# Kernel tuning notes

Hardware: AMD Instinct MI355X
Metric: run time of the kernel (lower is better)

The kernel has to match this reference:

```python
import jax, jax.numpy as jnp
import numpy as np

K_POOL = 5

def _conv_lookahead(x, W):
    # Faithful to F.conv2d(pad=(fs//2+1,0)) followed by keeping the last L rows:
    # for fs=3 this reduces to out[t] = sum_j x[t+j] @ W[:,j,:].T (2 trailing zeros).
    # x: [..., L, E], W: [nf, fs, E] -> out [..., L, nf]
    fs = W.shape[1]
    L = x.shape[-2]
    pad = [(0, 0)] * (x.ndim - 2) + [(0, fs - 1), (0, 0)]
    xp = jnp.pad(x, pad)
    out = sum(jnp.einsum('...le,fe->...lf', jax.lax.dynamic_slice_in_dim(xp, j, L, axis=-2), W[:, j, :]) for j in range(fs))
    return out

def _cosine(q, s):
    # q: [B,Q,D], s: [B,S,L,D] -> [B,S,Q,L]
    num = jnp.einsum('bqd,bsld->bsql', q, s)
    qn = jnp.linalg.norm(q, axis=-1)  # [B,Q]
    sn = jnp.linalg.norm(s, axis=-1)  # [B,S,L]
    return num / (qn[:, None, :, None] * sn[:, :, None, :])

def _pool(sim, k=K_POOL):
    # sort-based k-max pooling over last dim -> (max, mean-of-top-k), matching torch.sort + slice
    top = jax.lax.top_k(sim, k)[0]            # [..., Q, k] descending
    return jnp.stack([top[..., 0], top.mean(-1)], axis=-1)  # [..., Q, 2]

def _bce(p, t):
    return -(t * jnp.log(p) + (1.0 - t) * jnp.log(1.0 - p)).mean()

def setup_inputs() -> dict:
    key = jax.random.key(0)
    ks = jax.random.split(key, 9)
    B, S, L, Q, V, E, NF, FS = 16, 48, 64, 32, 50000, 300, 256, 3
    return {
        'sentences': jax.random.randint(ks[0], (B, S, L), 0, V, dtype=jnp.int64 if jax.config.jax_enable_x64 else jnp.int32).astype(jnp.int32),
        'question': jax.random.randint(ks[1], (B, Q), 0, V).astype(jnp.int32),
        'target_sents': jax.random.randint(ks[2], (B, S), 0, 2).astype(jnp.int32),
        'target_docs': jax.random.randint(ks[3], (B,), 0, 2).astype(jnp.int32),
        'similarity_one_hot': jax.random.uniform(ks[4], (B, S, Q, L), dtype=jnp.float32),
        'embeds': jax.random.normal(ks[5], (V, E), dtype=jnp.float32),
        'conv_w': jax.random.normal(ks[6], (NF, FS, E), dtype=jnp.float32),
        'lin_w': jax.random.normal(ks[7], (1, 6), dtype=jnp.float32),
        'lin_b': jax.random.normal(ks[8], (1,), dtype=jnp.float32),
    }

def reference(sentences, question, target_sents, target_docs, similarity_one_hot, embeds, conv_w, lin_w, lin_b):
    q_emb = embeds[question]            # [B,Q,E]
    s_emb = embeds[sentences]           # [B,S,L,E]
    q_conv = _conv_lookahead(q_emb, conv_w)   # [B,Q,NF]
    s_conv = _conv_lookahead(s_emb, conv_w)   # [B,S,L,NF]

    sim_ins = _cosine(q_emb, s_emb)     # [B,S,Q,L]
    qmask = (question > 1).astype(sim_ins.dtype)   # [B,Q]
    smask = (sentences > 1).astype(sim_ins.dtype)  # [B,S,L]
    sim_ins = sim_ins * qmask[:, None, :, None] * smask[:, :, None, :]

    sim_sens = _cosine(q_conv, s_conv)  # [B,S,Q,L]

    feats = jnp.concatenate([_pool(sim_ins), _pool(sim_sens), _pool(similarity_one_hot)], axis=-1)  # [B,S,Q,6]
    lo = jax.nn.sigmoid(jnp.einsum('bsqf,of->bsqo', feats, lin_w)[..., 0] + lin_b[0])  # [B,S,Q]
    sent_output = lo.mean(-1)           # [B,S]

    sal = _bce(sent_output, target_sents.astype(sent_output.dtype))
    doc_emit = sent_output.max(-1)      # [B]
    dal = _bce(doc_emit, target_docs.astype(doc_emit.dtype))
    total_loss = (sal + dal) / 2.0
    return (total_loss, sent_output, doc_emit)
```

## Files before the change

### kernel.cpp

```cpp
#include <hip/hip_runtime.h>
#include <math.h>

#define NB 16
#define NS 48
#define NL 64
#define NQ 32
#define NE 300
#define NF 256
#define KP 320
#define QROWS 36

typedef __attribute__((ext_vector_type(8))) short short8;
typedef __attribute__((ext_vector_type(4))) float f32x4;

#define MFMA(a,b,c) __builtin_amdgcn_mfma_f32_16x16x32_bf16((a),(b),(c),0,0,0)

__device__ __forceinline__ unsigned short f2bf(float f) {
    unsigned u = __float_as_uint(f);
    u += 0x7fff + ((u >> 16) & 1);
    return (unsigned short)(u >> 16);
}

__device__ __forceinline__ float wave_reduce_sum(float v) {
#pragma unroll
    for (int off = 32; off; off >>= 1) v += __shfl_xor(v, off, 64);
    return v;
}

__device__ __forceinline__ void top5_pool4(float v0, float v1, float v2, float v3,
                                           int lane, float* mx, float* mn) {
    float s0 = 0.f, s1 = 0.f, s2 = 0.f, s3 = 0.f;
    float x0 = 0.f, x1 = 0.f, x2 = 0.f, x3 = 0.f;
#pragma unroll
    for (int i = 0; i < 5; ++i) {
        float m0 = v0, m1 = v1, m2 = v2, m3 = v3;
#pragma unroll
        for (int off = 32; off; off >>= 1) {
            m0 = fmaxf(m0, __shfl_xor(m0, off, 64));
            m1 = fmaxf(m1, __shfl_xor(m1, off, 64));
            m2 = fmaxf(m2, __shfl_xor(m2, off, 64));
            m3 = fmaxf(m3, __shfl_xor(m3, off, 64));
        }
        if (i == 0) { x0 = m0; x1 = m1; x2 = m2; x3 = m3; }
        s0 += m0; s1 += m1; s2 += m2; s3 += m3;
        unsigned long long k0 = __ballot(v0 == m0);
        unsigned long long k1 = __ballot(v1 == m1);
        unsigned long long k2 = __ballot(v2 == m2);
        unsigned long long k3 = __ballot(v3 == m3);
        if (lane == __ffsll(k0) - 1) v0 = -3.4e38f;
        if (lane == __ffsll(k1) - 1) v1 = -3.4e38f;
        if (lane == __ffsll(k2) - 1) v2 = -3.4e38f;
        if (lane == __ffsll(k3) - 1) v3 = -3.4e38f;
    }
    mx[0] = x0; mx[1] = x1; mx[2] = x2; mx[3] = x3;
    mn[0] = s0 * 0.2f; mn[1] = s1 * 0.2f; mn[2] = s2 * 0.2f; mn[3] = s3 * 0.2f;
}

__global__ void wb2_kernel(const float* __restrict__ conv_w, short8* __restrict__ Wb2,
                           unsigned int* __restrict__ done_ctr,
                           float* __restrict__ qcssq) {
    if (blockIdx.x == 0 && threadIdx.x == 0) done_ctr[0] = 0u;
    int i = blockIdx.x * 256 + threadIdx.x;
    if (i < NB * NQ) qcssq[i] = 0.f;
    if (i >= 120 * 256) return;
    int rl = i & 15;
    int ftile = (i >> 4) & 15;
    int c = i >> 8;
    int kg = c & 3, rest = c >> 2;
    int ks = rest % 10, j = rest / 10;
    int f = ftile * 16 + rl;
    int k0 = ks * 32 + kg * 8;
    const float* src = conv_w + (size_t)(f * 3 + j) * NE;
    short8 h;
#pragma unroll
    for (int e = 0; e < 8; ++e) {
        int k = k0 + e;
        h[e] = (short)((k < NE) ? f2bf(src[k]) : (unsigned short)0);
    }
    Wb2[i] = h;
}

__global__ void qe_kernel(const int* __restrict__ question, const float* __restrict__ embeds,
                          unsigned short* __restrict__ qe, short8* __restrict__ qef,
                          float* __restrict__ q_norm) {
    int row = blockIdx.x;
    int b = row / QROWS, r = row % QROWS;
    int l = threadIdx.x;
    unsigned short* dst = qe + (size_t)row * KP;
    if (r < NQ) {
        int tok = question[b * NQ + r];
        const float4* rp = (const float4*)(embeds + (size_t)tok * NE);
        short8 h = {0, 0, 0, 0, 0, 0, 0, 0};
        float ss = 0.f;
        if (l < 38) {
            float4 v0 = rp[2 * l];
            ss += v0.x * v0.x + v0.y * v0.y + v0.z * v0.z + v0.w * v0.w;
            h[0] = (short)f2bf(v0.x); h[1] = (short)f2bf(v0.y);
            h[2] = (short)f2bf(v0.z); h[3] = (short)f2bf(v0.w);
            if (2 * l + 1 < 75) {
                float4 v1 = rp[2 * l + 1];
                ss += v1.x * v1.x + v1.y * v1.y + v1.z * v1.z + v1.w * v1.w;
                h[4] = (short)f2bf(v1.x); h[5] = (short)f2bf(v1.y);
                h[6] = (short)f2bf(v1.z); h[7] = (short)f2bf(v1.w);
            }
        }
        if (l < 40) {
            *(short8*)(dst + 8 * l) = h;
            qef[((size_t)(b * 2 + (r >> 4)) * 40 + l) * 16 + (r & 15)] = h;
        }
        ss = wave_reduce_sum(ss);
        if (l == 0) q_norm[b * NQ + r] = sqrtf(ss);
    } else {
        if (l < 40) {
            short8 z = {0, 0, 0, 0, 0, 0, 0, 0};
            *(short8*)(dst + 8 * l) = z;
        }
    }
}

__global__ __launch_bounds__(256) void qconv_mfma_kernel(
        const unsigned short* __restrict__ qe, const short8* __restrict__ Wb2,
        short8* __restrict__ qcf, float* __restrict__ qcssq) {
    __shared__ unsigned short tile[NQ][72];
    int b = blockIdx.x >> 2, fq = blockIdx.x & 3;
    int tid = threadIdx.x, lane = tid & 63, w = tid >> 6;
    int rl = lane & 15, kg = lane >> 4;
    int ftile = fq * 4 + w;
    f32x4 acc0 = (f32x4){0.f, 0.f, 0.f, 0.f};
    f32x4 acc1 = (f32x4){0.f, 0.f, 0.f, 0.f};
    for (int j = 0; j < 3; ++j) {
#pragma unroll 2
        for (int ks = 0; ks < 10; ++ks) {
            int k = ks * 32 + kg * 8;
            int c = (j * 10 + ks) * 4 + kg;
            short8 a0 = *(const short8*)(qe + ((size_t)(b * QROWS) + rl + j) * KP + k);
            short8 a1 = *(const short8*)(qe + ((size_t)(b * QROWS) + 16 + rl + j) * KP + k);
            short8 bb = Wb2[(c * 16 + ftile) * 16 + rl];
            acc0 = MFMA(a0, bb, acc0);
            acc1 = MFMA(a1, bb, acc1);
        }
    }
    int fl = w * 16 + rl;
#pragma unroll
    for (int reg = 0; reg < 4; ++reg) {
        tile[kg * 4 + reg][fl] = f2bf(acc0[reg]);
        tile[16 + kg * 4 + reg][fl] = f2bf(acc1[reg]);
    }
    __syncthreads();
    {
        int mh = tid >> 7, c_local = (tid >> 4) & 7, rl2 = tid & 15;
        short8 h = *(const short8*)(&tile[mh * 16 + rl2][c_local * 8]);
        qcf[((size_t)(b * 2 + mh) * 32 + 8 * fq + c_local) * 16 + rl2] = h;
    }
    {
        int qq = tid >> 3, fgrp = tid & 7;
        short8 h = *(const short8*)(&tile[qq][fgrp * 8]);
        float ss = 0.f;
#pragma unroll
        for (int e = 0; e < 8; ++e) {
            float v = __uint_as_float(((unsigned)(unsigned short)h[e]) << 16);
            ss += v * v;
        }
        ss += __shfl_xor(ss, 1, 64);
        ss += __shfl_xor(ss, 2, 64);
        ss += __shfl_xor(ss, 4, 64);
        if (fgrp == 0) atomicAdd(&qcssq[b * NQ + qq], ss);
    }
}

__global__ __launch_bounds__(256) void pack_kernel(
        const int* __restrict__ sentences, const float* __restrict__ embeds,
        short8* __restrict__ sB, float* __restrict__ snorm_g,
        float* __restrict__ scssq) {
    __shared__ unsigned short stg[16][328];
    __shared__ int toks[NL];
    int bs = blockIdx.x;
    int tid = threadIdx.x, lane = tid & 63, w = tid >> 6;
    if (tid < NL) {
        toks[tid] = sentences[(size_t)bs * NL + tid];
        scssq[bs * NL + tid] = 0.f;
    }
    __syncthreads();
    short8* sbb = sB + (size_t)bs * 40 * 64;
    for (int it = 0; it < 4; ++it) {
#pragma unroll
        for (int i = 0; i < 4; ++i) {
            int r16 = w * 4 + i;
            int r = it * 16 + r16;
            const float4* rp = (const float4*)(embeds + (size_t)toks[r] * NE);
            float ss;
            {
                float4 v = rp[lane];
                ss = v.x * v.x + v.y * v.y + v.z * v.z + v.w * v.w;
                ushort4 h = {f2bf(v.x), f2bf(v.y), f2bf(v.z), f2bf(v.w)};
                *(ushort4*)&stg[r16][4 * lane] = h;
            }
            if (lane < 11) {
                float4 v = rp[64 + lane];
                ss += v.x * v.x + v.y * v.y + v.z * v.z + v.w * v.w;
                ushort4 h = {f2bf(v.x), f2bf(v.y), f2bf(v.z), f2bf(v.w)};
                *(ushort4*)&stg[r16][256 + 4 * lane] = h;
            } else if (lane < 16) {
                ushort4 z = {0, 0, 0, 0};
                *(ushort4*)&stg[r16][256 + 4 * lane] = z;
            }
            ss = wave_reduce_sum(ss);
            if (lane == 0) snorm_g[bs * NL + r] = sqrtf(ss);
        }
        __syncthreads();
        {
            int c = tid >> 4, rl = tid & 15;
            for (; c < 40; c += 16) {
                short8 h = *(const short8*)&stg[rl][c * 8];
                sbb[(size_t)c * 64 + it * 16 + rl] = h;
            }
        }
        __syncthreads();
    }
}

__global__ __launch_bounds__(256) void ins_kernel(
        const int* __restrict__ sentences, const int* __restrict__ question,
        const short8* __restrict__ sB, const short8* __restrict__ qef,
        const float* __restrict__ snorm_g, const float* __restrict__ q_norm,
        float2* __restrict__ fpool_ins) {
    __shared__ float sim[NQ][66];
    __shared__ float qn_s[NQ], qmf_s[NQ];
    int bs = blockIdx.x, b = bs / NS;
    int tid = threadIdx.x, lane = tid & 63, w = tid >> 6;
    int rl = lane & 15, kg = lane >> 4;
    int t = (w << 4) + rl;
    if (tid < NQ) qn_s[tid] = q_norm[b * NQ + tid];
    else if (tid < 2 * NQ) {
        int q = tid - NQ;
        qmf_s[q] = (question[b * NQ + q] > 1) ? 1.f : 0.f;
    }
    float sn_t = snorm_g[bs * NL + t];
    float sm_t = (sentences[(size_t)bs * NL + t] > 1) ? 1.f : 0.f;
    __syncthreads();
    f32x4 i0 = (f32x4){0.f, 0.f, 0.f, 0.f};
    f32x4 i1 = (f32x4){0.f, 0.f, 0.f, 0.f};
    const short8* qf = qef + (size_t)(b * 80) * 16;
    const short8* sbb = sB + (size_t)bs * 40 * 64;
#pragma unroll 2
    for (int ks = 0; ks < 10; ++ks) {
        int c = ks * 4 + kg;
        short8 bB = sbb[(size_t)c * 64 + t];
        i0 = MFMA(qf[c * 16 + rl], bB, i0);
        i1 = MFMA(qf[(40 + c) * 16 + rl], bB, i1);
    }
    float inv_t = sm_t / sn_t;
#pragma unroll
    for (int reg = 0; reg < 4; ++reg) {
        int q0 = kg * 4 + reg;
        sim[q0][t] = i0[reg] / qn_s[q0] * inv_t * qmf_s[q0];
        int q1 = 16 + kg * 4 + reg;
        sim[q1][t] = i1[reg] / qn_s[q1] * inv_t * qmf_s[q1];
    }
    __syncthreads();
    int q0 = w << 3;
    float mx[4], mn[4];
    top5_pool4(sim[q0 + 0][lane], sim[q0 + 1][lane], sim[q0 + 2][lane], sim[q0 + 3][lane],
               lane, mx, mn);
    if (lane == 0)
#pragma unroll
        for (int p = 0; p < 4; ++p)
            fpool_ins[(size_t)bs * NQ + q0 + p] = (float2){mx[p], mn[p]};
    top5_pool4(sim[q0 + 4][lane], sim[q0 + 5][lane], sim[q0 + 6][lane], sim[q0 + 7][lane],
               lane, mx, mn);
    if (lane == 0)
#pragma unroll
        for (int p = 0; p < 4; ++p)
            fpool_ins[(size_t)bs * NQ + q0 + 4 + p] = (float2){mx[p], mn[p]};
}

__global__ __launch_bounds__(256) void conv_kernel(
        const short8* __restrict__ sB, const short8* __restrict__ Wb2,
        short8* __restrict__ scB, float* __restrict__ scssq) {
    __shared__ unsigned short scr[4][16][68];
    int bs = blockIdx.x;
    int tid = threadIdx.x, lane = tid & 63, w = tid >> 6;
    int rl = lane & 15, kg = lane >> 4;
    const short8* sbb = sB + (size_t)bs * 40 * 64;

    f32x4 cacc[4][4];
#pragma unroll
    for (int m = 0; m < 4; ++m)
#pragma unroll
        for (int nn = 0; nn < 4; ++nn) cacc[m][nn] = (f32x4){0.f, 0.f, 0.f, 0.f};

    for (int j = 0; j < 3; ++j) {
#pragma unroll 2
        for (int ks = 0; ks < 10; ++ks) {
            int cA = ks * 4 + kg;
            int c = (j * 10 + ks) * 4 + kg;
            short8 a[4], bb[4];
#pragma unroll
            for (int m = 0; m < 3; ++m)
                a[m] = sbb[(size_t)cA * 64 + m * 16 + rl + j];
            {
                int row3 = 48 + rl + j;
                short8 z = {0, 0, 0, 0, 0, 0, 0, 0};
                a[3] = (row3 < 64) ? sbb[(size_t)cA * 64 + row3] : z;
            }
#pragma unroll
            for (int nn = 0; nn < 4; ++nn)
                bb[nn] = Wb2[(c * 16 + (w * 4 + nn)) * 16 + rl];
#pragma unroll
            for (int m = 0; m < 4; ++m)
#pragma unroll
                for (int nn = 0; nn < 4; ++nn)
                    cacc[m][nn] = MFMA(a[m], bb[nn], cacc[m][nn]);
        }
    }

    short8* scb = scB + (size_t)bs * 32 * 64;
#pragma unroll
    for (int m = 0; m < 4; ++m) {
#pragma unroll
        for (int nn = 0; nn < 4; ++nn)
#pragma unroll
            for (int reg = 0; reg < 4; ++reg)
                scr[w][kg * 4 + reg][nn * 16 + rl] = f2bf(cacc[m][nn][reg]);
#pragma unroll
        for (int reg = 0; reg < 4; ++reg) {
            float ss = 0.f;
#pragma unroll
            for (int nn = 0; nn < 4; ++nn) {
                float v = cacc[m][nn][reg];
                ss += v * v;
            }
            ss += __shfl_xor(ss, 1, 64);
            ss += __shfl_xor(ss, 2, 64);
            ss += __shfl_xor(ss, 4, 64);
            ss += __shfl_xor(ss, 8, 64);
            if (rl == 0) atomicAdd(&scssq[bs * NL + m * 16 + kg * 4 + reg], ss);
        }
#pragma unroll
        for (int p = 0; p < 2; ++p) {
            int cl = (lane >> 4) + p * 4;
            int rl2 = lane & 15;
            short8 v = *(const short8*)&scr[w][rl2][cl * 8];
            scb[(size_t)(w * 8 + cl) * 64 + m * 16 + rl2] = v;
        }
    }
}

__global__ __launch_bounds__(256) void sens_kernel(
        const float* __restrict__ sim_oh,
        const short8* __restrict__ scB, const short8* __restrict__ qcf,
        const float* __restrict__ qcssq, const float* __restrict__ scssq,
        const float2* __restrict__ fpool_ins,
        const float* __restrict__ lin_w, const float* __restrict__ lin_b,
        const int* __restrict__ tsent, const int* __restrict__ tdoc,
        unsigned int* __restrict__ done_ctr,
        float* __restrict__ sent_ws, float* __restrict__ d_out) {
    __shared__ float sim[NQ][66];
    __shared__ float qcn_s[NQ];
    __shared__ float wq[4];
    __shared__ int lastflag;
    __shared__ float red2[4];
    __shared__ float dred[NB];
    int bs = blockIdx.x, b = bs / NS;
    int tid = threadIdx.x, lane = tid & 63, w = tid >> 6;
    int rl = lane & 15, kg = lane >> 4;
    int t = (w << 4) + rl;
    if (tid < NQ) qcn_s[tid] = sqrtf(qcssq[b * NQ + tid]);
    float scn_t = sqrtf(scssq[bs * NL + t]);
    float oh[8];
#pragma unroll
    for (int qi = 0; qi < 8; ++qi) {
        int q = (w << 3) + qi;
        oh[qi] = sim_oh[((size_t)bs * NQ + q) * NL + lane];
    }
    f32x4 sacc0 = (f32x4){0.f, 0.f, 0.f, 0.f};
    f32x4 sacc1 = (f32x4){0.f, 0.f, 0.f, 0.f};
    const short8* qc = qcf + (size_t)(b * 64) * 16;
    const short8* scb = scB + (size_t)bs * 32 * 64;
#pragma unroll 2
    for (int ks = 0; ks < 8; ++ks) {
        int c = ks * 4 + kg;
        short8 bB = scb[(size_t)c * 64 + t];
        sacc0 = MFMA(qc[c * 16 + rl], bB, sacc0);
        sacc1 = MFMA(qc[(32 + c) * 16 + rl], bB, sacc1);
    }
    __syncthreads();
    float inv_t = 1.f / scn_t;
#pragma unroll
    for (int reg = 0; reg < 4; ++reg) {
        int q0 = kg * 4 + reg;
        sim[q0][t] = sacc0[reg] / qcn_s[q0] * inv_t;
        int q1 = 16 + kg * 4 + reg;
        sim[q1][t] = sacc1[reg] / qcn_s[q1] * inv_t;
    }
    __syncthreads();

    {
        float lw0 = lin_w[0], lw1 = lin_w[1], lw2 = lin_w[2];
        float lw3 = lin_w[3], lw4 = lin_w[4], lw5 = lin_w[5];
        float lb = lin_b[0];
        int q0 = w << 3;
        float mxs[8], mns[8], mxo[8], mno[8];
        top5_pool4(sim[q0 + 0][lane], sim[q0 + 1][lane], sim[q0 + 2][lane],
                   sim[q0 + 3][lane], lane, mxs, mns);
        top5_pool4(sim[q0 + 4][lane], sim[q0 + 5][lane], sim[q0 + 6][lane],
                   sim[q0 + 7][lane], lane, mxs + 4, mns + 4);
        top5_pool4(oh[0], oh[1], oh[2], oh[3], lane, mxo, mno);
        top5_pool4(oh[4], oh[5], oh[6], oh[7], lane, mxo + 4, mno + 4);
        float psum = 0.f;
#pragma unroll
        for (int qi = 0; qi < 8; ++qi) {
            float2 fp = fpool_ins[(size_t)bs * NQ + q0 + qi];
            float z = fp.x * lw0 + fp.y * lw1 + mxs[qi] * lw2 + mns[qi] * lw3 +
                      mxo[qi] * lw4 + mno[qi] * lw5 + lb;
            psum += 1.f / (1.f + expf(-z));
        }
        if (lane == 0) wq[w] = psum;
    }
    __syncthreads();
    if (tid == 0) {
        float sent = (wq[0] + wq[1] + wq[2] + wq[3]) * (1.f / 32.f);
        __hip_atomic_store(&sent_ws[bs], sent, __ATOMIC_RELEASE, __HIP_MEMORY_SCOPE_AGENT);
        d_out[1 + bs] = sent;
        unsigned old = atomicAdd(done_ctr, 1u);
        lastflag = (old == (unsigned)(NB * NS - 1)) ? 1 : 0;
    }
    __syncthreads();

    if (lastflag) {
        float acc_l = 0.f;
        for (int i = tid; i < NB * NS; i += 256) {
            float p = __hip_atomic_load(&sent_ws[i], __ATOMIC_ACQUIRE, __HIP_MEMORY_SCOPE_AGENT);
            float tt2 = (float)tsent[i];
            acc_l += tt2 * logf(p) + (1.f - tt2) * logf(1.f - p);
        }
        acc_l = wave_reduce_sum(acc_l);
        if ((tid & 63) == 0) red2[tid >> 6] = acc_l;
        if (tid < NB) {
            float m = -3.4e38f;
            for (int s = 0; s < NS; ++s)
                m = fmaxf(m, __hip_atomic_load(&sent_ws[tid * NS + s], __ATOMIC_ACQUIRE,
                                               __HIP_MEMORY_SCOPE_AGENT));
            d_out[1 + NB * NS + tid] = m;
            float tt2 = (float)tdoc[tid];
            dred[tid] = tt2 * logf(m) + (1.f - tt2) * logf(1.f - m);
        }
        __syncthreads();
        if (tid == 0) {
            float sal = -(red2[0] + red2[1] + red2[2] + red2[3]) / (float)(NB * NS);
            float dsum = 0.f;
            for (int i = 0; i < NB; ++i) dsum += dred[i];
            float dal = -dsum / (float)NB;
            d_out[0] = 0.5f * (sal + dal);
        }
    }
}

extern "C" void kernel_launch(void* const* d_in, const int* in_sizes, int n_in,
                              void* d_out, int out_size, void* d_ws, size_t ws_size,
                              hipStream_t stream) {
    const int* sentences = (const int*)d_in[0];
    const int* question = (const int*)d_in[1];
    const int* tsent = (const int*)d_in[2];
    const int* tdoc = (const int*)d_in[3];
    const float* sim_oh = (const float*)d_in[4];
    const float* embeds = (const float*)d_in[5];
    const float* conv_w = (const float*)d_in[6];
    const float* lin_w = (const float*)d_in[7];
    const float* lin_b = (const float*)d_in[8];
    float* out = (float*)d_out;

    char* wsc = (char*)d_ws;
    short8* Wb2            = (short8*)(wsc);
    unsigned short* qe_old = (unsigned short*)(wsc + 491520);
    short8* qef            = (short8*)(wsc + 860160);
    short8* qcf            = (short8*)(wsc + 1187840);
    float* q_norm          = (float*)(wsc + 1449984);
    float* qcssq           = (float*)(wsc + 1452032);
    float* sent_ws         = (float*)(wsc + 1454080);
    unsigned int* done_ctr = (unsigned int*)(wsc + 1457152);
    float* snorm_g         = (float*)(wsc + 1457168);
    float* scssq           = (float*)(wsc + 1653776);
    float2* fpool_ins      = (float2*)(wsc + 1850384);
    short8* sB             = (short8*)(wsc + 2046992);
    short8* scB            = (short8*)(wsc + 33504272);

    wb2_kernel<<<120, 256, 0, stream>>>(conv_w, Wb2, done_ctr, qcssq);
    qe_kernel<<<NB * QROWS, 64, 0, stream>>>(question, embeds, qe_old, qef, q_norm);
    qconv_mfma_kernel<<<NB * 4, 256, 0, stream>>>(qe_old, Wb2, qcf, qcssq);
    pack_kernel<<<NB * NS, 256, 0, stream>>>(sentences, embeds, sB, snorm_g, scssq);
    ins_kernel<<<NB * NS, 256, 0, stream>>>(sentences, question, sB, qef,
                                            snorm_g, q_norm, fpool_ins);
    conv_kernel<<<NB * NS, 256, 0, stream>>>(sB, Wb2, scB, scssq);
    sens_kernel<<<NB * NS, 256, 0, stream>>>(
        sim_oh, scB, qcf, qcssq, scssq, fpool_ins,
        lin_w, lin_b, tsent, tdoc, done_ctr, sent_ws, out);
}
```

Measured before the change: 135.9 us.

## Split ins, conv and sens kernels across two blocks per sentence

Each of the three per-sentence kernels now launches two blocks per sentence. For ins and sens, each block handles half of the question rows; for conv, each block handles half of the output filters. The goal is to fill more of the GPU's compute units with smaller per-block work. In exchange, sentence outputs are built from partial sums with float atomics into a buffer that must be zeroed first, the completion counter now targets twice the block count, and the A-operand loads in conv are duplicated across the two halves.

```diff
diff --git a/kernel.cpp b/kernel.cpp
--- a/kernel.cpp
+++ b/kernel.cpp
@@ -58,10 +58,11 @@
 
 __global__ void wb2_kernel(const float* __restrict__ conv_w, short8* __restrict__ Wb2,
                            unsigned int* __restrict__ done_ctr,
-                           float* __restrict__ qcssq) {
+                           float* __restrict__ qcssq, float* __restrict__ sent_ws) {
     if (blockIdx.x == 0 && threadIdx.x == 0) done_ctr[0] = 0u;
     int i = blockIdx.x * 256 + threadIdx.x;
     if (i < NB * NQ) qcssq[i] = 0.f;
+    if (i < NB * NS) sent_ws[i] = 0.f;
     if (i >= 120 * 256) return;
     int rl = i & 15;
     int ftile = (i >> 4) & 15;
@@ -224,77 +225,68 @@
         const short8* __restrict__ sB, const short8* __restrict__ qef,
         const float* __restrict__ snorm_g, const float* __restrict__ q_norm,
         float2* __restrict__ fpool_ins) {
-    __shared__ float sim[NQ][66];
-    __shared__ float qn_s[NQ], qmf_s[NQ];
-    int bs = blockIdx.x, b = bs / NS;
+    __shared__ float sim[16][66];
+    __shared__ float qn_s[16], qmf_s[16];
+    int bs = blockIdx.x >> 1, qh = blockIdx.x & 1;
+    int b = bs / NS;
     int tid = threadIdx.x, lane = tid & 63, w = tid >> 6;
     int rl = lane & 15, kg = lane >> 4;
     int t = (w << 4) + rl;
-    if (tid < NQ) qn_s[tid] = q_norm[b * NQ + tid];
-    else if (tid < 2 * NQ) {
-        int q = tid - NQ;
-        qmf_s[q] = (question[b * NQ + q] > 1) ? 1.f : 0.f;
+    if (tid < 16) qn_s[tid] = q_norm[b * NQ + qh * 16 + tid];
+    else if (tid < 32) {
+        int q = tid - 16;
+        qmf_s[q] = (question[b * NQ + qh * 16 + q] > 1) ? 1.f : 0.f;
     }
     float sn_t = snorm_g[bs * NL + t];
     float sm_t = (sentences[(size_t)bs * NL + t] > 1) ? 1.f : 0.f;
     __syncthreads();
     f32x4 i0 = (f32x4){0.f, 0.f, 0.f, 0.f};
-    f32x4 i1 = (f32x4){0.f, 0.f, 0.f, 0.f};
-    const short8* qf = qef + (size_t)(b * 80) * 16;
+    const short8* qf = qef + (size_t)((b * 2 + qh) * 40) * 16;
     const short8* sbb = sB + (size_t)bs * 40 * 64;
 #pragma unroll 2
     for (int ks = 0; ks < 10; ++ks) {
         int c = ks * 4 + kg;
         short8 bB = sbb[(size_t)c * 64 + t];
         i0 = MFMA(qf[c * 16 + rl], bB, i0);
-        i1 = MFMA(qf[(40 + c) * 16 + rl], bB, i1);
     }
     float inv_t = sm_t / sn_t;
 #pragma unroll
     for (int reg = 0; reg < 4; ++reg) {
-        int q0 = kg * 4 + reg;
-        sim[q0][t] = i0[reg] / qn_s[q0] * inv_t * qmf_s[q0];
-        int q1 = 16 + kg * 4 + reg;
-        sim[q1][t] = i1[reg] / qn_s[q1] * inv_t * qmf_s[q1];
-    }
-    __syncthreads();
-    int q0 = w << 3;
+        int ql = kg * 4 + reg;
+        sim[ql][t] = i0[reg] / qn_s[ql] * inv_t * qmf_s[ql];
+    }
+    __syncthreads();
+    int ql0 = w << 2;
     float mx[4], mn[4];
-    top5_pool4(sim[q0 + 0][lane], sim[q0 + 1][lane], sim[q0 + 2][lane], sim[q0 + 3][lane],
-               lane, mx, mn);
+    top5_pool4(sim[ql0 + 0][lane], sim[ql0 + 1][lane], sim[ql0 + 2][lane],
+               sim[ql0 + 3][lane], lane, mx, mn);
     if (lane == 0)
 #pragma unroll
         for (int p = 0; p < 4; ++p)
-            fpool_ins[(size_t)bs * NQ + q0 + p] = (float2){mx[p], mn[p]};
-    top5_pool4(sim[q0 + 4][lane], sim[q0 + 5][lane], sim[q0 + 6][lane], sim[q0 + 7][lane],
-               lane, mx, mn);
-    if (lane == 0)
-#pragma unroll
-        for (int p = 0; p < 4; ++p)
-            fpool_ins[(size_t)bs * NQ + q0 + 4 + p] = (float2){mx[p], mn[p]};
+            fpool_ins[(size_t)bs * NQ + qh * 16 + ql0 + p] = (float2){mx[p], mn[p]};
 }
 
 __global__ __launch_bounds__(256) void conv_kernel(
         const short8* __restrict__ sB, const short8* __restrict__ Wb2,
         short8* __restrict__ scB, float* __restrict__ scssq) {
-    __shared__ unsigned short scr[4][16][68];
-    int bs = blockIdx.x;
+    __shared__ unsigned short scr[4][16][40];
+    int bs = blockIdx.x >> 1, fh = blockIdx.x & 1;
     int tid = threadIdx.x, lane = tid & 63, w = tid >> 6;
     int rl = lane & 15, kg = lane >> 4;
     const short8* sbb = sB + (size_t)bs * 40 * 64;
 
-    f32x4 cacc[4][4];
+    f32x4 cacc[4][2];
 #pragma unroll
     for (int m = 0; m < 4; ++m)
 #pragma unroll
-        for (int nn = 0; nn < 4; ++nn) cacc[m][nn] = (f32x4){0.f, 0.f, 0.f, 0.f};
+        for (int nn = 0; nn < 2; ++nn) cacc[m][nn] = (f32x4){0.f, 0.f, 0.f, 0.f};
 
     for (int j = 0; j < 3; ++j) {
 #pragma unroll 2
         for (int ks = 0; ks < 10; ++ks) {
             int cA = ks * 4 + kg;
             int c = (j * 10 + ks) * 4 + kg;
-            short8 a[4], bb[4];
+            short8 a[4], bb[2];
 #pragma unroll
             for (int m = 0; m < 3; ++m)
                 a[m] = sbb[(size_t)cA * 64 + m * 16 + rl + j];
@@ -304,12 +296,12 @@
                 a[3] = (row3 < 64) ? sbb[(size_t)cA * 64 + row3] : z;
             }
 #pragma unroll
-            for (int nn = 0; nn < 4; ++nn)
-                bb[nn] = Wb2[(c * 16 + (w * 4 + nn)) * 16 + rl];
+            for (int nn = 0; nn < 2; ++nn)
+                bb[nn] = Wb2[(c * 16 + (fh * 8 + w * 2 + nn)) * 16 + rl];
 #pragma unroll
             for (int m = 0; m < 4; ++m)
 #pragma unroll
-                for (int nn = 0; nn < 4; ++nn)
+                for (int nn = 0; nn < 2; ++nn)
                     cacc[m][nn] = MFMA(a[m], bb[nn], cacc[m][nn]);
         }
     }
@@ -318,7 +310,7 @@
 #pragma unroll
     for (int m = 0; m < 4; ++m) {
 #pragma unroll
-        for (int nn = 0; nn < 4; ++nn)
+        for (int nn = 0; nn < 2; ++nn)
 #pragma unroll
             for (int reg = 0; reg < 4; ++reg)
                 scr[w][kg * 4 + reg][nn * 16 + rl] = f2bf(cacc[m][nn][reg]);
@@ -326,7 +318,7 @@
         for (int reg = 0; reg < 4; ++reg) {
             float ss = 0.f;
 #pragma unroll
-            for (int nn = 0; nn < 4; ++nn) {
+            for (int nn = 0; nn < 2; ++nn) {
                 float v = cacc[m][nn][reg];
                 ss += v * v;
             }
@@ -336,12 +328,11 @@
             ss += __shfl_xor(ss, 8, 64);
             if (rl == 0) atomicAdd(&scssq[bs * NL + m * 16 + kg * 4 + reg], ss);
         }
-#pragma unroll
-        for (int p = 0; p < 2; ++p) {
-            int cl = (lane >> 4) + p * 4;
+        {
+            int cl = lane >> 4;
             int rl2 = lane & 15;
             short8 v = *(const short8*)&scr[w][rl2][cl * 8];
-            scb[(size_t)(w * 8 + cl) * 64 + m * 16 + rl2] = v;
+            scb[(size_t)(fh * 16 + w * 4 + cl) * 64 + m * 16 + rl2] = v;
         }
     }
 }
@@ -355,43 +346,40 @@
         const int* __restrict__ tsent, const int* __restrict__ tdoc,
         unsigned int* __restrict__ done_ctr,
         float* __restrict__ sent_ws, float* __restrict__ d_out) {
-    __shared__ float sim[NQ][66];
-    __shared__ float qcn_s[NQ];
+    __shared__ float sim[16][66];
+    __shared__ float qcn_s[16];
     __shared__ float wq[4];
     __shared__ int lastflag;
     __shared__ float red2[4];
     __shared__ float dred[NB];
-    int bs = blockIdx.x, b = bs / NS;
+    int bs = blockIdx.x >> 1, qh = blockIdx.x & 1;
+    int b = bs / NS;
     int tid = threadIdx.x, lane = tid & 63, w = tid >> 6;
     int rl = lane & 15, kg = lane >> 4;
     int t = (w << 4) + rl;
-    if (tid < NQ) qcn_s[tid] = sqrtf(qcssq[b * NQ + tid]);
+    if (tid < 16) qcn_s[tid] = sqrtf(qcssq[b * NQ + qh * 16 + tid]);
     float scn_t = sqrtf(scssq[bs * NL + t]);
-    float oh[8];
-#pragma unroll
-    for (int qi = 0; qi < 8; ++qi) {
-        int q = (w << 3) + qi;
+    float oh[4];
+#pragma unroll
+    for (int qi = 0; qi < 4; ++qi) {
+        int q = qh * 16 + (w << 2) + qi;
         oh[qi] = sim_oh[((size_t)bs * NQ + q) * NL + lane];
     }
     f32x4 sacc0 = (f32x4){0.f, 0.f, 0.f, 0.f};
-    f32x4 sacc1 = (f32x4){0.f, 0.f, 0.f, 0.f};
-    const short8* qc = qcf + (size_t)(b * 64) * 16;
+    const short8* qc = qcf + (size_t)((b * 2 + qh) * 32) * 16;
     const short8* scb = scB + (size_t)bs * 32 * 64;
 #pragma unroll 2
     for (int ks = 0; ks < 8; ++ks) {
         int c = ks * 4 + kg;
         short8 bB = scb[(size_t)c * 64 + t];
         sacc0 = MFMA(qc[c * 16 + rl], bB, sacc0);
-        sacc1 = MFMA(qc[(32 + c) * 16 + rl], bB, sacc1);
     }
     __syncthreads();
     float inv_t = 1.f / scn_t;
 #pragma unroll
     for (int reg = 0; reg < 4; ++reg) {
-        int q0 = kg * 4 + reg;
-        sim[q0][t] = sacc0[reg] / qcn_s[q0] * inv_t;
-        int q1 = 16 + kg * 4 + reg;
-        sim[q1][t] = sacc1[reg] / qcn_s[q1] * inv_t;
+        int ql = kg * 4 + reg;
+        sim[ql][t] = sacc0[reg] / qcn_s[ql] * inv_t;
     }
     __syncthreads();
 
@@ -399,18 +387,15 @@
         float lw0 = lin_w[0], lw1 = lin_w[1], lw2 = lin_w[2];
         float lw3 = lin_w[3], lw4 = lin_w[4], lw5 = lin_w[5];
         float lb = lin_b[0];
-        int q0 = w << 3;
-        float mxs[8], mns[8], mxo[8], mno[8];
-        top5_pool4(sim[q0 + 0][lane], sim[q0 + 1][lane], sim[q0 + 2][lane],
-                   sim[q0 + 3][lane], lane, mxs, mns);
-        top5_pool4(sim[q0 + 4][lane], sim[q0 + 5][lane], sim[q0 + 6][lane],
-                   sim[q0 + 7][lane], lane, mxs + 4, mns + 4);
+        int ql0 = w << 2;
+        float mxs[4], mns[4], mxo[4], mno[4];
+        top5_pool4(sim[ql0 + 0][lane], sim[ql0 + 1][lane], sim[ql0 + 2][lane],
+                   sim[ql0 + 3][lane], lane, mxs, mns);
         top5_pool4(oh[0], oh[1], oh[2], oh[3], lane, mxo, mno);
-        top5_pool4(oh[4], oh[5], oh[6], oh[7], lane, mxo + 4, mno + 4);
         float psum = 0.f;
 #pragma unroll
-        for (int qi = 0; qi < 8; ++qi) {
-            float2 fp = fpool_ins[(size_t)bs * NQ + q0 + qi];
+        for (int qi = 0; qi < 4; ++qi) {
+            float2 fp = fpool_ins[(size_t)bs * NQ + qh * 16 + ql0 + qi];
             float z = fp.x * lw0 + fp.y * lw1 + mxs[qi] * lw2 + mns[qi] * lw3 +
                       mxo[qi] * lw4 + mno[qi] * lw5 + lb;
             psum += 1.f / (1.f + expf(-z));
@@ -419,11 +404,11 @@
     }
     __syncthreads();
     if (tid == 0) {
-        float sent = (wq[0] + wq[1] + wq[2] + wq[3]) * (1.f / 32.f);
-        __hip_atomic_store(&sent_ws[bs], sent, __ATOMIC_RELEASE, __HIP_MEMORY_SCOPE_AGENT);
-        d_out[1 + bs] = sent;
-        unsigned old = atomicAdd(done_ctr, 1u);
-        lastflag = (old == (unsigned)(NB * NS - 1)) ? 1 : 0;
+        float partial = (wq[0] + wq[1] + wq[2] + wq[3]) * (1.f / 32.f);
+        atomicAdd(&sent_ws[bs], partial);
+        unsigned old = __hip_atomic_fetch_add(done_ctr, 1u, __ATOMIC_ACQ_REL,
+                                              __HIP_MEMORY_SCOPE_AGENT);
+        lastflag = (old == (unsigned)(2 * NB * NS - 1)) ? 1 : 0;
     }
     __syncthreads();
 
@@ -431,6 +416,7 @@
         float acc_l = 0.f;
         for (int i = tid; i < NB * NS; i += 256) {
             float p = __hip_atomic_load(&sent_ws[i], __ATOMIC_ACQUIRE, __HIP_MEMORY_SCOPE_AGENT);
+            d_out[1 + i] = p;
             float tt2 = (float)tsent[i];
             acc_l += tt2 * logf(p) + (1.f - tt2) * logf(1.f - p);
         }
@@ -485,14 +471,14 @@
     short8* sB             = (short8*)(wsc + 2046992);
     short8* scB            = (short8*)(wsc + 33504272);
 
-    wb2_kernel<<<120, 256, 0, stream>>>(conv_w, Wb2, done_ctr, qcssq);
+    wb2_kernel<<<120, 256, 0, stream>>>(conv_w, Wb2, done_ctr, qcssq, sent_ws);
     qe_kernel<<<NB * QROWS, 64, 0, stream>>>(question, embeds, qe_old, qef, q_norm);
     qconv_mfma_kernel<<<NB * 4, 256, 0, stream>>>(qe_old, Wb2, qcf, qcssq);
     pack_kernel<<<NB * NS, 256, 0, stream>>>(sentences, embeds, sB, snorm_g, scssq);
-    ins_kernel<<<NB * NS, 256, 0, stream>>>(sentences, question, sB, qef,
-                                            snorm_g, q_norm, fpool_ins);
-    conv_kernel<<<NB * NS, 256, 0, stream>>>(sB, Wb2, scB, scssq);
-    sens_kernel<<<NB * NS, 256, 0, stream>>>(
+    ins_kernel<<<NB * NS * 2, 256, 0, stream>>>(sentences, question, sB, qef,
+                                                snorm_g, q_norm, fpool_ins);
+    conv_kernel<<<NB * NS * 2, 256, 0, stream>>>(sB, Wb2, scB, scssq);
+    sens_kernel<<<NB * NS * 2, 256, 0, stream>>>(
         sim_oh, scB, qcf, qcssq, scssq, fpool_ins,
         lin_w, lin_b, tsent, tdoc, done_ctr, sent_ws, out);
 }
```

Result: slower. 162.5 us (+19.6%).
